# Optimization experiments

Hardware: AMD Instinct MI355X
Metric: run time of the kernel (lower is better)

The kernel has to match this reference:

```python
import jax, jax.numpy as jnp
import numpy as np

H, DK, DV = 16, 64, 64  # head_nums, key_size, head_size
D_MODEL = H * DK        # 1024
OUT_DIM = H * DV        # 1024


def setup_inputs() -> dict:
    key = jax.random.key(0)
    ks = jax.random.split(key, 12)
    B, S = 2, 2048
    scale = 0.02
    return {
        "q": jax.random.normal(ks[0], (B, S, D_MODEL), jnp.float32),
        "k": jax.random.normal(ks[1], (B, S, D_MODEL), jnp.float32),
        "v": jax.random.normal(ks[2], (B, S, D_MODEL), jnp.float32),
        "Wq": jax.random.normal(ks[3], (D_MODEL, H * DK), jnp.float32) * scale,
        "bq": jnp.zeros((H * DK,), jnp.float32),
        "Wk": jax.random.normal(ks[4], (D_MODEL, H * DK), jnp.float32) * scale,
        "bk": jnp.zeros((H * DK,), jnp.float32),
        "Wv": jax.random.normal(ks[5], (D_MODEL, OUT_DIM), jnp.float32) * scale,
        "bv": jnp.zeros((OUT_DIM,), jnp.float32),
        "Wo": jax.random.normal(ks[6], (OUT_DIM, OUT_DIM), jnp.float32) * scale,
        "bo": jnp.zeros((OUT_DIM,), jnp.float32),
    }


def reference(q, k, v, Wq, bq, Wk, bk, Wv, bv, Wo, bo):
    B, S, _ = q.shape
    # linear projections, split heads
    qw = (q @ Wq + bq).reshape(B, S, H, DK)   # [B,S,H,dk]
    kw = (k @ Wk + bk).reshape(B, S, H, DK)   # [B,S,H,dk]
    vw = (v @ Wv + bv).reshape(B, S, H, DV)   # [B,S,H,dv]
    # scaled dot-product attention scores
    att = jnp.einsum("bshk,bqhk->bhsq", qw, kw) / (DK ** 0.5)  # [B,H,S,S]
    att = jax.nn.softmax(att, axis=-1)
    out = jnp.einsum("bhsq,bqhk->bhsk", att, vw)  # [B,H,S,dv]
    out = out.transpose(0, 2, 1, 3).reshape(B, S, OUT_DIM)  # merge heads
    return out @ Wo + bo
```

## Files before the change

kernel.cpp:

```cpp
#include <hip/hip_runtime.h>
#include <hip/hip_bf16.h>

#define BB 2
#define SS 2048
#define HH 16
#define DD 64
#define DM 1024
#define MM (BB*SS)

typedef __attribute__((ext_vector_type(4))) float f32x4;
typedef __attribute__((ext_vector_type(16))) float f32x16;
typedef __attribute__((ext_vector_type(8))) short s16x8;
typedef __attribute__((ext_vector_type(2))) int i32x2;

__device__ __forceinline__ unsigned short f2bf(float f){
  unsigned int u = __float_as_uint(f);
  u += 0x7FFF + ((u >> 16) & 1);
  return (unsigned short)(u >> 16);
}

__device__ __forceinline__ f32x4 zero4(){ f32x4 z = {0.f,0.f,0.f,0.f}; return z; }

__device__ __forceinline__ unsigned int cvtpk(float a, float b){
  unsigned int r;
  asm("v_cvt_pk_bf16_f32 %0, %1, %2" : "=v"(r) : "v"(a), "v"(b));
  return r;
}

__device__ __forceinline__ void gload_lds16(const void* g, void* l){
  __builtin_amdgcn_global_load_lds(
    (const __attribute__((address_space(1))) unsigned int*)g,
    (__attribute__((address_space(3))) unsigned int*)l, 16, 0, 0);
}

__global__ __launch_bounds__(256) void wtrans_kernel(
    const float* __restrict__ Wq, const float* __restrict__ Wk,
    const float* __restrict__ Wv, const float* __restrict__ Wo,
    short* __restrict__ wt){
  __shared__ float tile[64][65];
  const float* src = (blockIdx.y==0)?Wq:(blockIdx.y==1)?Wk:(blockIdx.y==2)?Wv:Wo;
  short* dst = wt + (size_t)blockIdx.y * ((size_t)DM*DM);
  int tk = (blockIdx.x >> 4) * 64;
  int tn = (blockIdx.x & 15) * 64;
  int t = threadIdx.x;
  int r = t >> 2;
  int c4 = (t & 3) << 4;
  const float* p = src + (size_t)(tk + r) * DM + tn + c4;
  #pragma unroll
  for (int i = 0; i < 4; ++i){
    float4 vv = *(const float4*)(p + i*4);
    tile[r][c4 + i*4 + 0] = vv.x;
    tile[r][c4 + i*4 + 1] = vv.y;
    tile[r][c4 + i*4 + 2] = vv.z;
    tile[r][c4 + i*4 + 3] = vv.w;
  }
  __syncthreads();
  s16x8 o0, o1;
  #pragma unroll
  for (int j = 0; j < 8; ++j) o0[j] = (short)f2bf(tile[c4 + j][r]);
  #pragma unroll
  for (int j = 0; j < 8; ++j) o1[j] = (short)f2bf(tile[c4 + 8 + j][r]);
  short* qd = dst + (size_t)(tn + r) * DM + tk + c4;
  *(s16x8*)qd       = o0;
  *(s16x8*)(qd + 8) = o1;
}


#define ALOAD_F32(k0_) { \
  _Pragma("unroll") for (int ch=0; ch<4; ++ch){ \
    areg[2*ch]   = *(const float4*)(Apf + (size_t)ch*32*DM + (k0_)); \
    areg[2*ch+1] = *(const float4*)(Apf + (size_t)ch*32*DM + (k0_) + 4); \
  } }

#define AWRITE(AB_) { \
  _Pragma("unroll") for (int ch=0; ch<4; ++ch){ \
    int4 pk4; \
    pk4.x = (int)cvtpk(areg[2*ch].x,   areg[2*ch].y); \
    pk4.y = (int)cvtpk(areg[2*ch].z,   areg[2*ch].w); \
    pk4.z = (int)cvtpk(areg[2*ch+1].x, areg[2*ch+1].y); \
    pk4.w = (int)cvtpk(areg[2*ch+1].z, areg[2*ch+1].w); \
    *(int4*)((char*)(AB_) + ch*4096 + adst) = pk4; \
  } }

#define ASTAGE_BF16(k0_, AB_) { \
  gload_lds16(Apb + (k0_),          (char*)(AB_) + w*1024); \
  gload_lds16(Apb + 32*DM + (k0_),  (char*)(AB_) + 4096  + w*1024); \
  gload_lds16(Apb + 64*DM + (k0_),  (char*)(AB_) + 8192  + w*1024); \
  gload_lds16(Apb + 96*DM + (k0_),  (char*)(AB_) + 12288 + w*1024); \
}

#define GEMM_PRE_COMMON() \
  int m0 = blockIdx.x * 128, n0 = blockIdx.y * 64; \
  int t = threadIdx.x; \
  int w = t >> 6, lane = t & 63, g = lane >> 4, c = lane & 15; \
  int wm = (w >> 1) * 64, wn = (w & 1) * 32; \
  f32x4 acc[4][2]; \
  _Pragma("unroll") for (int i=0;i<4;++i) \
    _Pragma("unroll") for (int j=0;j<2;++j) acc[i][j] = zero4(); \
  int srow = t >> 3; \
  int scol = ((t & 7) ^ (srow & 7)) * 8; \
  const short* Bp = BT + (size_t)(n0 + srow) * DM + scol; \
  int rsw = (c & 7) << 4; \
  int adst = srow*128 + (t & 7)*16;

#define BSTAGE(k0_, BB_) { \
  gload_lds16(Bp + (k0_),          (char*)(BB_) + w*1024); \
  gload_lds16(Bp + 32*DM + (k0_),  (char*)(BB_) + 4096 + w*1024); \
}

#define GCOMP(AB_, BB_) { \
  s16x8 af[4][2], bfr[2][2]; \
  _Pragma("unroll") for (int mi=0;mi<4;++mi){ \
    const char* arow = (const char*)(AB_) + (wm + mi*16 + c)*128; \
    af[mi][0] = *(const s16x8*)(arow + ((g*16) ^ rsw)); \
    af[mi][1] = *(const s16x8*)(arow + ((64 + g*16) ^ rsw)); \
  } \
  _Pragma("unroll") for (int ni=0;ni<2;++ni){ \
    const char* brow = (const char*)(BB_) + (wn + ni*16 + c)*128; \
    bfr[ni][0] = *(const s16x8*)(brow + ((g*16) ^ rsw)); \
    bfr[ni][1] = *(const s16x8*)(brow + ((64 + g*16) ^ rsw)); \
  } \
  _Pragma("unroll") for (int mi=0;mi<4;++mi) \
    _Pragma("unroll") for (int ni=0;ni<2;++ni){ \
      acc[mi][ni] = __builtin_amdgcn_mfma_f32_16x16x32_bf16(af[mi][0], bfr[ni][0], acc[mi][ni], 0,0,0); \
      acc[mi][ni] = __builtin_amdgcn_mfma_f32_16x16x32_bf16(af[mi][1], bfr[ni][1], acc[mi][ni], 0,0,0); \
    } \
}

#define GEMM_LOOP_BF16() \
  ASTAGE_BF16(0, &As[0][0]) \
  BSTAGE(0, &Bs[0][0]) \
  __syncthreads(); \
  for (int kk = 0; kk < DM; kk += 128){ \
    if (kk + 64 < DM){ ASTAGE_BF16(kk+64, &As[1][0]) BSTAGE(kk+64, &Bs[1][0]) } \
    GCOMP(&As[0][0], &Bs[0][0]) \
    __syncthreads(); \
    if (kk + 128 < DM){ ASTAGE_BF16(kk+128, &As[0][0]) BSTAGE(kk+128, &Bs[0][0]) } \
    GCOMP(&As[1][0], &Bs[1][0]) \
    __syncthreads(); \
  }

#define GEMM_PRE_128() \
  int m0 = blockIdx.x * 128, n0 = blockIdx.y * 128; \
  int t = threadIdx.x; \
  int w = t >> 6, lane = t & 63, g = lane >> 4, c = lane & 15; \
  int wm = (w >> 1) * 64, wn = (w & 1) * 64; \
  f32x4 acc[4][4]; \
  _Pragma("unroll") for (int i=0;i<4;++i) \
    _Pragma("unroll") for (int j=0;j<4;++j) acc[i][j] = zero4(); \
  int srow = t >> 3; \
  int scol = ((t & 7) ^ (srow & 7)) * 8; \
  const short* Bp = BT + (size_t)(n0 + srow) * DM + scol; \
  int rsw = (c & 7) << 4; \
  int adst = srow*128 + (t & 7)*16;

#define BSTAGE128(k0_, BB_) { \
  gload_lds16(Bp + (k0_),          (char*)(BB_) + w*1024); \
  gload_lds16(Bp + 32*DM + (k0_),  (char*)(BB_) + 4096  + w*1024); \
  gload_lds16(Bp + 64*DM + (k0_),  (char*)(BB_) + 8192  + w*1024); \
  gload_lds16(Bp + 96*DM + (k0_),  (char*)(BB_) + 12288 + w*1024); \
}

#define GCOMP128(AB_, BB_) { \
  s16x8 af[4][2], bfr[4][2]; \
  _Pragma("unroll") for (int mi=0;mi<4;++mi){ \
    const char* arow = (const char*)(AB_) + (wm + mi*16 + c)*128; \
    af[mi][0] = *(const s16x8*)(arow + ((g*16) ^ rsw)); \
    af[mi][1] = *(const s16x8*)(arow + ((64 + g*16) ^ rsw)); \
  } \
  _Pragma("unroll") for (int ni=0;ni<4;++ni){ \
    const char* brow = (const char*)(BB_) + (wn + ni*16 + c)*128; \
    bfr[ni][0] = *(const s16x8*)(brow + ((g*16) ^ rsw)); \
    bfr[ni][1] = *(const s16x8*)(brow + ((64 + g*16) ^ rsw)); \
  } \
  _Pragma("unroll") for (int mi=0;mi<4;++mi) \
    _Pragma("unroll") for (int ni=0;ni<4;++ni){ \
      acc[mi][ni] = __builtin_amdgcn_mfma_f32_16x16x32_bf16(af[mi][0], bfr[ni][0], acc[mi][ni], 0,0,0); \
      acc[mi][ni] = __builtin_amdgcn_mfma_f32_16x16x32_bf16(af[mi][1], bfr[ni][1], acc[mi][ni], 0,0,0); \
    } \
}

#define GEMM_LOOP_F32_128() \
  float4 areg[8]; \
  ALOAD_F32(0) \
  BSTAGE128(0, &Bs[0][0]) \
  AWRITE(&As[0][0]) \
  __syncthreads(); \
  for (int kk = 0; kk < DM; kk += 128){ \
    if (kk + 64 < DM){ ALOAD_F32(kk+64) BSTAGE128(kk+64, &Bs[1][0]) } \
    GCOMP128(&As[0][0], &Bs[0][0]) \
    if (kk + 64 < DM){ AWRITE(&As[1][0]) } \
    __syncthreads(); \
    if (kk + 128 < DM){ ALOAD_F32(kk+128) BSTAGE128(kk+128, &Bs[0][0]) } \
    GCOMP128(&As[1][0], &Bs[1][0]) \
    if (kk + 128 < DM){ AWRITE(&As[0][0]) } \
    __syncthreads(); \
  }

__global__ __launch_bounds__(256) void gemm_qkv3_kernel(
    const float* __restrict__ qs, const float* __restrict__ ks,
    const float* __restrict__ vs, const short* __restrict__ WT3,
    const float* __restrict__ bq, const float* __restrict__ bk,
    const float* __restrict__ bv,
    short* __restrict__ Qh, short* __restrict__ Kh, short* __restrict__ Vt,
    float qscale){
  __shared__ __align__(16) short As[2][128*64];
  __shared__ __align__(16) short Bs[2][128*64];
  int z = blockIdx.z;
  const float* A    = (z==0) ? qs : (z==1) ? ks : vs;
  const short* BT   = WT3 + (size_t)z * ((size_t)DM*DM);
  const float* bias = (z==0) ? bq : (z==1) ? bk : bv;
  GEMM_PRE_128()
  const float* Apf = A + (size_t)(m0 + srow) * DM + scol;
  GEMM_LOOP_F32_128()
  if (z < 2){
    short* outh = (z==0) ? Qh : Kh;
    float scale = (z==0) ? qscale : 1.0f;
    #pragma unroll
    for (int ni=0;ni<4;++ni){
      int col = n0 + wn + ni*16 + c;
      float bvv = bias[col];
      int hh = col >> 6, d = col & 63;
      #pragma unroll
      for (int mi=0;mi<4;++mi){
        #pragma unroll
        for (int r=0;r<4;++r){
          int row = m0 + wm + mi*16 + g*4 + r;
          int b = row >> 11, s = row & (SS-1);
          float val = (acc[mi][ni][r] + bvv) * scale;
          outh[((((size_t)b*HH + hh)*SS + s) << 6) + d] = (short)f2bf(val);
        }
      }
    }
  } else {
    #pragma unroll
    for (int ni=0;ni<4;++ni){
      int col = n0 + wn + ni*16 + c;
      float bvv = bias[col];
      int hh = col >> 6, d = col & 63;
      #pragma unroll
      for (int mi=0;mi<4;++mi){
        int row = m0 + wm + mi*16 + g*4;
        int b = row >> 11, s = row & (SS-1);
        i32x2 pk2;
        pk2.x = (int)cvtpk(acc[mi][ni][0] + bvv, acc[mi][ni][1] + bvv);
        pk2.y = (int)cvtpk(acc[mi][ni][2] + bvv, acc[mi][ni][3] + bvv);
        *(i32x2*)(Vt + (((size_t)(b*HH + hh)*64 + d) * SS + s)) = pk2;
      }
    }
  }
}

__global__ __launch_bounds__(256) void gemm_out_kernel(
    const short* __restrict__ A, const short* __restrict__ BT,
    const float* __restrict__ bias, float* __restrict__ out){
  __shared__ __align__(16) short As[2][128*64];
  __shared__ __align__(16) short Bs[2][64*64];
  GEMM_PRE_COMMON()
  const short* Apb = A + (size_t)(m0 + srow) * DM + scol;
  GEMM_LOOP_BF16()
  #pragma unroll
  for (int ni=0;ni<2;++ni){
    int col = n0 + wn + ni*16 + c;
    float bvv = bias[col];
    #pragma unroll
    for (int mi=0;mi<4;++mi){
      #pragma unroll
      for (int r=0;r<4;++r){
        int row = m0 + wm + mi*16 + g*4 + r;
        out[(size_t)row * DM + col] = acc[mi][ni][r] + bvv;
      }
    }
  }
}

__global__ __launch_bounds__(256) void attn_kernel(
    const short* __restrict__ Qh, const short* __restrict__ Kh,
    const short* __restrict__ Vt, short* __restrict__ Oh){
  __shared__ __align__(16) short SMEM[16384];
  int n = blockIdx.x + (blockIdx.y << 4);
  int bh = (n & 7) | ((n >> 7) << 3);
  int qb = ((n >> 3) & 15) * 128;
  int t = threadIdx.x, w = t >> 6, lane = t & 63;
  int lq = lane & 31, h = lane >> 5;
  int qrow0 = qb + w*32;

  const short* qg = Qh + (((size_t)bh*SS + qrow0 + lq) << 6) + h*8;
  s16x8 qf[4];
  #pragma unroll
  for (int kc=0;kc<4;++kc) qf[kc] = *(const s16x8*)(qg + kc*16);

  f32x16 z16;
  #pragma unroll
  for (int i=0;i<16;++i) z16[i] = 0.f;
  f32x16 oA, oB;
  #pragma unroll
  for (int i=0;i<16;++i){ oA[i]=0.f; oB[i]=0.f; }
  float l = 0.f;
  const char* kbase = (const char*)(Kh + (((size_t)bh*SS) << 6));
  const char* vbase = (const char*)(Vt + ((size_t)bh*64) * SS);

  int rsel = lane >> 3;
  int csw  = ((lane & 7) << 4) ^ (rsel << 4);
  int swr  = (lane & 7) << 4;

  const char* smem = (const char*)&SMEM[0];
  const char* kr0 = smem + lq*128 + (( 0 + h*16) ^ swr);
  const char* kr1 = smem + lq*128 + ((32 + h*16) ^ swr);
  const char* kr2 = smem + lq*128 + ((64 + h*16) ^ swr);
  const char* kr3 = smem + lq*128 + ((96 + h*16) ^ swr);
  char* smem_w = (char*)&SMEM[0] + w*2048;

#define STAGE(T, BOFF) { \
    const char* kg = kbase + (((size_t)((T)*64 + w*16 + rsel)) << 7) + csw; \
    gload_lds16(kg,        smem_w + (BOFF)); \
    gload_lds16(kg + 1024, smem_w + (BOFF) + 1024); \
    const char* vg = vbase + (size_t)(w*16 + rsel) * (SS*2) + ((size_t)(T) << 7) + csw; \
    gload_lds16(vg,            smem_w + (BOFF) + 16384); \
    gload_lds16(vg + 8*(SS*2), smem_w + (BOFF) + 16384 + 1024); \
  }

#define MFMA32(a_, b_, c_) __builtin_amdgcn_mfma_f32_32x32x16_bf16(a_, b_, c_, 0,0,0)

#define TILE(BOFF) { \
    f32x16 sA, sB; \
    s16x8 kf; \
    __builtin_amdgcn_s_setprio(1); \
    kf = *(const s16x8*)(kr0 + (BOFF));        sA = MFMA32(kf, qf[0], z16); \
    kf = *(const s16x8*)(kr0 + (BOFF) + 4096); sB = MFMA32(kf, qf[0], z16); \
    kf = *(const s16x8*)(kr1 + (BOFF));        sA = MFMA32(kf, qf[1], sA); \
    kf = *(const s16x8*)(kr1 + (BOFF) + 4096); sB = MFMA32(kf, qf[1], sB); \
    kf = *(const s16x8*)(kr2 + (BOFF));        sA = MFMA32(kf, qf[2], sA); \
    kf = *(const s16x8*)(kr2 + (BOFF) + 4096); sB = MFMA32(kf, qf[2], sB); \
    kf = *(const s16x8*)(kr3 + (BOFF));        sA = MFMA32(kf, qf[3], sA); \
    kf = *(const s16x8*)(kr3 + (BOFF) + 4096); sB = MFMA32(kf, qf[3], sB); \
    __builtin_amdgcn_s_setprio(0); \
    float lp = 0.f; \
    unsigned int cA[8], cB[8]; \
    _Pragma("unroll") \
    for (int i=0;i<8;++i){ \
      float a0 = __builtin_amdgcn_exp2f(sA[2*i]); \
      float a1 = __builtin_amdgcn_exp2f(sA[2*i+1]); \
      float b0 = __builtin_amdgcn_exp2f(sB[2*i]); \
      float b1 = __builtin_amdgcn_exp2f(sB[2*i+1]); \
      lp += (a0 + a1) + (b0 + b1); \
      cA[i] = cvtpk(a0, a1); \
      cB[i] = cvtpk(b0, b1); \
    } \
    l += lp; \
    asm("v_permlane32_swap_b32 %0, %1" : "+v"(cA[0]), "+v"(cA[2])); \
    asm("v_permlane32_swap_b32 %0, %1" : "+v"(cA[1]), "+v"(cA[3])); \
    asm("v_permlane32_swap_b32 %0, %1" : "+v"(cA[4]), "+v"(cA[6])); \
    asm("v_permlane32_swap_b32 %0, %1" : "+v"(cA[5]), "+v"(cA[7])); \
    asm("v_permlane32_swap_b32 %0, %1" : "+v"(cB[0]), "+v"(cB[2])); \
    asm("v_permlane32_swap_b32 %0, %1" : "+v"(cB[1]), "+v"(cB[3])); \
    asm("v_permlane32_swap_b32 %0, %1" : "+v"(cB[4]), "+v"(cB[6])); \
    asm("v_permlane32_swap_b32 %0, %1" : "+v"(cB[5]), "+v"(cB[7])); \
    s16x8 pbf0, pbf1, pbf2, pbf3; \
    { unsigned int* p0 = (unsigned int*)&pbf0; \
      p0[0]=cA[0]; p0[1]=cA[1]; p0[2]=cA[2]; p0[3]=cA[3]; \
      unsigned int* p1 = (unsigned int*)&pbf1; \
      p1[0]=cA[4]; p1[1]=cA[5]; p1[2]=cA[6]; p1[3]=cA[7]; \
      unsigned int* p2 = (unsigned int*)&pbf2; \
      p2[0]=cB[0]; p2[1]=cB[1]; p2[2]=cB[2]; p2[3]=cB[3]; \
      unsigned int* p3 = (unsigned int*)&pbf3; \
      p3[0]=cB[4]; p3[1]=cB[5]; p3[2]=cB[6]; p3[3]=cB[7]; } \
    __builtin_amdgcn_s_setprio(1); \
    kf = *(const s16x8*)(kr0 + (BOFF) + 16384);        oA = MFMA32(kf, pbf0, oA); \
    kf = *(const s16x8*)(kr0 + (BOFF) + 16384 + 4096); oB = MFMA32(kf, pbf0, oB); \
    kf = *(const s16x8*)(kr1 + (BOFF) + 16384);        oA = MFMA32(kf, pbf1, oA); \
    kf = *(const s16x8*)(kr1 + (BOFF) + 16384 + 4096); oB = MFMA32(kf, pbf1, oB); \
    kf = *(const s16x8*)(kr2 + (BOFF) + 16384);        oA = MFMA32(kf, pbf2, oA); \
    kf = *(const s16x8*)(kr2 + (BOFF) + 16384 + 4096); oB = MFMA32(kf, pbf2, oB); \
    kf = *(const s16x8*)(kr3 + (BOFF) + 16384);        oA = MFMA32(kf, pbf3, oA); \
    kf = *(const s16x8*)(kr3 + (BOFF) + 16384 + 4096); oB = MFMA32(kf, pbf3, oB); \
    __builtin_amdgcn_s_setprio(0); \
  }

  STAGE(0, 0)
  __syncthreads();

  for (int tb = 0; tb < 32; tb += 2){
    STAGE(tb+1, 8192)
    TILE(0)
    __syncthreads();
    if (tb + 2 < 32) STAGE(tb+2, 0)
    TILE(8192)
    __syncthreads();
  }
#undef STAGE
#undef TILE

  l += __shfl_xor(l, 32);
  float inv = 1.f / l;
  int b = bh >> 4, hh = bh & 15;
  short* ob = Oh + (((size_t)(b*SS + qrow0 + lq)) << 10) + hh*64 + 4*h;
  #pragma unroll
  for (int rg=0;rg<4;++rg){
    i32x2 pk;
    pk.x = (int)cvtpk(oA[rg*4+0]*inv, oA[rg*4+1]*inv);
    pk.y = (int)cvtpk(oA[rg*4+2]*inv, oA[rg*4+3]*inv);
    *(i32x2*)(ob + 8*rg) = pk;
    pk.x = (int)cvtpk(oB[rg*4+0]*inv, oB[rg*4+1]*inv);
    pk.y = (int)cvtpk(oB[rg*4+2]*inv, oB[rg*4+3]*inv);
    *(i32x2*)(ob + 32 + 8*rg) = pk;
  }
}

extern "C" void kernel_launch(void* const* d_in, const int* in_sizes, int n_in,
                              void* d_out, int out_size, void* d_ws, size_t ws_size,
                              hipStream_t stream){
  const float* q  = (const float*)d_in[0];
  const float* k  = (const float*)d_in[1];
  const float* v  = (const float*)d_in[2];
  const float* Wq = (const float*)d_in[3];
  const float* bq = (const float*)d_in[4];
  const float* Wk = (const float*)d_in[5];
  const float* bk = (const float*)d_in[6];
  const float* Wv = (const float*)d_in[7];
  const float* bv = (const float*)d_in[8];
  const float* Wo = (const float*)d_in[9];
  const float* bo = (const float*)d_in[10];
  (void)in_sizes; (void)n_in; (void)out_size; (void)ws_size;

  short* wsp = (short*)d_ws;
  const size_t MW = 1048576;
  short* WT3 = wsp;
  short* WTo = wsp + 3*MW;
  short* Qh  = wsp + 4*MW;
  short* Kh  = wsp + 8*MW;
  short* Oh  = wsp + 12*MW;
  short* Vt  = wsp + 16*MW;

  const float QSCALE = 0.125f * 1.44269504088896f;
  wtrans_kernel<<<dim3(256,4), 256, 0, stream>>>(Wq, Wk, Wv, Wo, wsp);
  gemm_qkv3_kernel<<<dim3(32,8,3), 256, 0, stream>>>(q, k, v, WT3, bq, bk, bv,
                                                     Qh, Kh, Vt, QSCALE);
  attn_kernel<<<dim3(16,32), 256, 0, stream>>>(Qh, Kh, Vt, Oh);
  gemm_out_kernel<<<dim3(32,16), 256, 0, stream>>>(Oh, WTo, bo, (float*)d_out);
}
```

Measured before the change: 116.8 us.

## Stage two K/V tiles per barrier in attention with doubled LDS buffers

The attention kernel's LDS buffer is doubled to 64KB so two K/V tiles are loaded per stage. Each barrier interval now computes two tiles, which halves the number of __syncthreads and puts more load latency behind each compute phase. The cost is twice the LDS per block, which may lower occupancy (blocks per CU).

```diff
diff --git a/kernel.cpp b/kernel.cpp
--- a/kernel.cpp
+++ b/kernel.cpp
@@ -64,7 +64,6 @@
   *(s16x8*)qd       = o0;
   *(s16x8*)(qd + 8) = o1;
 }
-
 
 #define ALOAD_F32(k0_) { \
   _Pragma("unroll") for (int ch=0; ch<4; ++ch){ \
@@ -277,7 +276,7 @@
 __global__ __launch_bounds__(256) void attn_kernel(
     const short* __restrict__ Qh, const short* __restrict__ Kh,
     const short* __restrict__ Vt, short* __restrict__ Oh){
-  __shared__ __align__(16) short SMEM[16384];
+  __shared__ __align__(16) short SMEM[32768];
   int n = blockIdx.x + (blockIdx.y << 4);
   int bh = (n & 7) | ((n >> 7) << 3);
   int qb = ((n >> 3) & 15) * 128;
@@ -311,29 +310,29 @@
   const char* kr3 = smem + lq*128 + ((96 + h*16) ^ swr);
   char* smem_w = (char*)&SMEM[0] + w*2048;
 
-#define STAGE(T, BOFF) { \
+#define STAGE(T, KOFF) { \
     const char* kg = kbase + (((size_t)((T)*64 + w*16 + rsel)) << 7) + csw; \
-    gload_lds16(kg,        smem_w + (BOFF)); \
-    gload_lds16(kg + 1024, smem_w + (BOFF) + 1024); \
+    gload_lds16(kg,        smem_w + (KOFF)); \
+    gload_lds16(kg + 1024, smem_w + (KOFF) + 1024); \
     const char* vg = vbase + (size_t)(w*16 + rsel) * (SS*2) + ((size_t)(T) << 7) + csw; \
-    gload_lds16(vg,            smem_w + (BOFF) + 16384); \
-    gload_lds16(vg + 8*(SS*2), smem_w + (BOFF) + 16384 + 1024); \
+    gload_lds16(vg,            smem_w + (KOFF) + 32768); \
+    gload_lds16(vg + 8*(SS*2), smem_w + (KOFF) + 32768 + 1024); \
   }
 
 #define MFMA32(a_, b_, c_) __builtin_amdgcn_mfma_f32_32x32x16_bf16(a_, b_, c_, 0,0,0)
 
-#define TILE(BOFF) { \
+#define TILE(KOFF) { \
     f32x16 sA, sB; \
     s16x8 kf; \
     __builtin_amdgcn_s_setprio(1); \
-    kf = *(const s16x8*)(kr0 + (BOFF));        sA = MFMA32(kf, qf[0], z16); \
-    kf = *(const s16x8*)(kr0 + (BOFF) + 4096); sB = MFMA32(kf, qf[0], z16); \
-    kf = *(const s16x8*)(kr1 + (BOFF));        sA = MFMA32(kf, qf[1], sA); \
-    kf = *(const s16x8*)(kr1 + (BOFF) + 4096); sB = MFMA32(kf, qf[1], sB); \
-    kf = *(const s16x8*)(kr2 + (BOFF));        sA = MFMA32(kf, qf[2], sA); \
-    kf = *(const s16x8*)(kr2 + (BOFF) + 4096); sB = MFMA32(kf, qf[2], sB); \
-    kf = *(const s16x8*)(kr3 + (BOFF));        sA = MFMA32(kf, qf[3], sA); \
-    kf = *(const s16x8*)(kr3 + (BOFF) + 4096); sB = MFMA32(kf, qf[3], sB); \
+    kf = *(const s16x8*)(kr0 + (KOFF));        sA = MFMA32(kf, qf[0], z16); \
+    kf = *(const s16x8*)(kr0 + (KOFF) + 4096); sB = MFMA32(kf, qf[0], z16); \
+    kf = *(const s16x8*)(kr1 + (KOFF));        sA = MFMA32(kf, qf[1], sA); \
+    kf = *(const s16x8*)(kr1 + (KOFF) + 4096); sB = MFMA32(kf, qf[1], sB); \
+    kf = *(const s16x8*)(kr2 + (KOFF));        sA = MFMA32(kf, qf[2], sA); \
+    kf = *(const s16x8*)(kr2 + (KOFF) + 4096); sB = MFMA32(kf, qf[2], sB); \
+    kf = *(const s16x8*)(kr3 + (KOFF));        sA = MFMA32(kf, qf[3], sA); \
+    kf = *(const s16x8*)(kr3 + (KOFF) + 4096); sB = MFMA32(kf, qf[3], sB); \
     __builtin_amdgcn_s_setprio(0); \
     float lp = 0.f; \
     unsigned int cA[8], cB[8]; \
@@ -366,26 +365,31 @@
       unsigned int* p3 = (unsigned int*)&pbf3; \
       p3[0]=cB[4]; p3[1]=cB[5]; p3[2]=cB[6]; p3[3]=cB[7]; } \
     __builtin_amdgcn_s_setprio(1); \
-    kf = *(const s16x8*)(kr0 + (BOFF) + 16384);        oA = MFMA32(kf, pbf0, oA); \
-    kf = *(const s16x8*)(kr0 + (BOFF) + 16384 + 4096); oB = MFMA32(kf, pbf0, oB); \
-    kf = *(const s16x8*)(kr1 + (BOFF) + 16384);        oA = MFMA32(kf, pbf1, oA); \
-    kf = *(const s16x8*)(kr1 + (BOFF) + 16384 + 4096); oB = MFMA32(kf, pbf1, oB); \
-    kf = *(const s16x8*)(kr2 + (BOFF) + 16384);        oA = MFMA32(kf, pbf2, oA); \
-    kf = *(const s16x8*)(kr2 + (BOFF) + 16384 + 4096); oB = MFMA32(kf, pbf2, oB); \
-    kf = *(const s16x8*)(kr3 + (BOFF) + 16384);        oA = MFMA32(kf, pbf3, oA); \
-    kf = *(const s16x8*)(kr3 + (BOFF) + 16384 + 4096); oB = MFMA32(kf, pbf3, oB); \
+    kf = *(const s16x8*)(kr0 + (KOFF) + 32768);        oA = MFMA32(kf, pbf0, oA); \
+    kf = *(const s16x8*)(kr0 + (KOFF) + 32768 + 4096); oB = MFMA32(kf, pbf0, oB); \
+    kf = *(const s16x8*)(kr1 + (KOFF) + 32768);        oA = MFMA32(kf, pbf1, oA); \
+    kf = *(const s16x8*)(kr1 + (KOFF) + 32768 + 4096); oB = MFMA32(kf, pbf1, oB); \
+    kf = *(const s16x8*)(kr2 + (KOFF) + 32768);        oA = MFMA32(kf, pbf2, oA); \
+    kf = *(const s16x8*)(kr2 + (KOFF) + 32768 + 4096); oB = MFMA32(kf, pbf2, oB); \
+    kf = *(const s16x8*)(kr3 + (KOFF) + 32768);        oA = MFMA32(kf, pbf3, oA); \
+    kf = *(const s16x8*)(kr3 + (KOFF) + 32768 + 4096); oB = MFMA32(kf, pbf3, oB); \
     __builtin_amdgcn_s_setprio(0); \
   }
 
   STAGE(0, 0)
+  STAGE(1, 8192)
   __syncthreads();
 
-  for (int tb = 0; tb < 32; tb += 2){
-    STAGE(tb+1, 8192)
+  for (int tb = 0; tb < 32; tb += 4){
+    if (tb + 2 < 32) STAGE(tb+2, 16384)
+    if (tb + 3 < 32) STAGE(tb+3, 24576)
     TILE(0)
+    TILE(8192)
     __syncthreads();
-    if (tb + 2 < 32) STAGE(tb+2, 0)
-    TILE(8192)
+    if (tb + 4 < 32) STAGE(tb+4, 0)
+    if (tb + 5 < 32) STAGE(tb+5, 8192)
+    TILE(16384)
+    TILE(24576)
     __syncthreads();
   }
 #undef STAGE
```

Result: no change. 115.8 us (-0.8%).
